# Performance work log

Measured on AMD Instinct MI355X. Metric: run time of the kernel, lower is better.

Reference implementation:

```python
import jax, jax.numpy as jnp
import numpy as np
from functools import partial

N_NODES = 50000


def gcn_conv(x, row, col, norm, W, b, num_nodes):
    # x: [N, Fin], W: [Fout, Fin] (torch Linear weight layout), b: [Fout]
    h = x @ W.T                                   # [N, Fout]
    msg = norm[:, None] * h[row]                  # per-edge message, gather x_j = x[row]
    out = jax.ops.segment_sum(msg, col, num_segments=num_nodes)  # scatter-add to target col
    return out + b


def _build_norm(row, col, edge_weight, num_nodes):
    # add self-loops with weight 1.0
    loops = jnp.arange(num_nodes, dtype=row.dtype)
    row_f = jnp.concatenate([row, loops])
    col_f = jnp.concatenate([col, loops])
    ew_f = jnp.concatenate([edge_weight, jnp.ones((num_nodes,), edge_weight.dtype)])
    # degree counts occurrences of row (unweighted, like PyG degree())
    deg = jax.ops.segment_sum(jnp.ones_like(ew_f), row_f, num_segments=num_nodes)
    dinv = jnp.where(deg > 0, deg ** -0.5, 0.0).astype(edge_weight.dtype)
    norm = dinv[row_f] * ew_f * dinv[col_f]
    return row_f, col_f, norm


def setup_inputs() -> dict:
    key = jax.random.key(0)
    k = jax.random.split(key, 8)
    N, E = N_NODES, 800000
    Fin, H, C = 256, 96, 40
    x = jax.random.normal(k[0], (N, Fin), dtype=jnp.float32)
    edge_index = jax.random.randint(k[1], (2, E), 0, N, dtype=jnp.int64)
    edge_weight = jax.random.uniform(k[2], (E,), dtype=jnp.float32)
    W1 = jax.random.normal(k[3], (H, Fin), dtype=jnp.float32) * (1.0 / np.sqrt(Fin))
    b1 = jnp.zeros((H,), jnp.float32)
    W2 = jax.random.normal(k[4], (C, H), dtype=jnp.float32) * (1.0 / np.sqrt(H))
    b2 = jnp.zeros((C,), jnp.float32)
    return {"x": x, "edge_index": edge_index, "edge_weight": edge_weight,
            "W1": W1, "b1": b1, "W2": W2, "b2": b2}


def reference(x, edge_index, edge_weight, W1, b1, W2, b2):
    N = x.shape[0]
    row, col = edge_index[0], edge_index[1]
    row_f, col_f, norm = _build_norm(row, col, edge_weight, N)
    h = jax.nn.relu(gcn_conv(x, row_f, col_f, norm, W1, b1, N))
    # dropout is identity in eval mode
    out = gcn_conv(h, row_f, col_f, norm, W2, b2, N)
    return jax.nn.log_softmax(out, axis=1)
```

## Files before the change

kernel.cpp:

```cpp
#include <hip/hip_runtime.h>
#include <hip/hip_bf16.h>
#include <hip/hip_fp16.h>
#include <math.h>

#define NN 50000
#define EE 800000
#define FIN 256
#define FH 96
#define FC 40
#define NBK 196

typedef _Float16 h4 __attribute__((ext_vector_type(4)));
typedef _Float16 h8 __attribute__((ext_vector_type(8)));
typedef float f32x4 __attribute__((ext_vector_type(4)));


__global__ __launch_bounds__(256) void k_hist(const int* __restrict__ ei, int E,
                                              unsigned* __restrict__ copies) {
    __shared__ unsigned hist[12500];
    int b = blockIdx.x;
    int slice = b & 63;
    int half = (b >> 6) & 1;
    int arr = b >> 7;
    const int* ptr = ei + (size_t)arr * E;
    int tid = threadIdx.x;
    for (int i = tid; i < 12500; i += 256) hist[i] = 0u;
    __syncthreads();
    int ES = (E + 63) >> 6;
    int lo = slice * ES, hi = min(lo + ES, E);
    int nlo = half * 25000;
    for (int i = lo + tid; i < hi; i += 256) {
        int rel = ptr[i] - nlo;
        if ((unsigned)rel < 25000u)
            atomicAdd(&hist[rel >> 1], 1u << ((rel & 1) << 4));
    }
    __syncthreads();
    unsigned* dst = copies + (size_t)((arr * 2 + half) * 64 + slice) * 12500;
    for (int i = tid; i < 12500; i += 256) dst[i] = hist[i];
}

__global__ void k_reduce(const unsigned* __restrict__ copies,
                         float* __restrict__ dinv, unsigned* __restrict__ cnt) {
    int t = blockIdx.x * blockDim.x + threadIdx.x;
    if (t >= 25000) return;
    int half = t / 12500, w = t - half * 12500;
    unsigned sr = 0, sc = 0;
    const unsigned* br = copies + (size_t)(half) * 64 * 12500 + w;
    const unsigned* bc = copies + (size_t)(2 + half) * 64 * 12500 + w;
#pragma unroll 8
    for (int s = 0; s < 64; ++s) { sr += br[s * 12500]; sc += bc[s * 12500]; }
    int n0 = half * 25000 + 2 * w;
    dinv[n0]     = rsqrtf((float)((sr & 0xffffu) + 1u));
    dinv[n0 + 1] = rsqrtf((float)((sr >> 16) + 1u));
    cnt[n0]     = sc & 0xffffu;
    cnt[n0 + 1] = sc >> 16;
}


__global__ __launch_bounds__(1024) void k_scanA(const unsigned* __restrict__ cnt,
                                                unsigned* __restrict__ off,
                                                unsigned* __restrict__ bsum, int n) {
    __shared__ unsigned s[1024];
    int t = threadIdx.x;
    int i = blockIdx.x * 1024 + t;
    unsigned v = (i < n) ? cnt[i] : 0u;
    s[t] = v;
    __syncthreads();
    for (int o = 1; o < 1024; o <<= 1) {
        unsigned tv = (t >= o) ? s[t - o] : 0u;
        __syncthreads();
        s[t] += tv;
        __syncthreads();
    }
    if (i < n) off[i] = s[t] - v;
    if (t == 1023) bsum[blockIdx.x] = s[1023];
}

__global__ void k_scanB1(unsigned* bsum, int nb) {
    if (threadIdx.x == 0 && blockIdx.x == 0) {
        unsigned run = 0;
        for (int b = 0; b < nb; ++b) { unsigned tv = bsum[b]; bsum[b] = run; run += tv; }
    }
}

__global__ void k_scanB2(unsigned* __restrict__ off, const unsigned* __restrict__ bsum,
                         unsigned* __restrict__ gcur, int n, unsigned e) {
    int i = blockIdx.x * blockDim.x + threadIdx.x;
    if (i < n) {
        unsigned v = off[i] + bsum[i >> 10];
        off[i] = v;
        if ((i & 255) == 0) gcur[i >> 8] = v;
    }
    if (i == n) off[n] = e;
}


__global__ __launch_bounds__(256) void k_bucket(const int* __restrict__ row,
                                                const int* __restrict__ col,
                                                const float* __restrict__ ew,
                                                unsigned* __restrict__ gcur,
                                                unsigned* __restrict__ bkc,
                                                float2* __restrict__ bkrw, int E) {
    __shared__ unsigned cnt[NBK];
    __shared__ unsigned cur[NBK];
    int tid = threadIdx.x;
    int CH = (E + gridDim.x - 1) / gridDim.x;
    int lo = blockIdx.x * CH, hi = min(lo + CH, E);
    for (int i = tid; i < NBK; i += 256) cnt[i] = 0u;
    __syncthreads();
    for (int i = lo + tid; i < hi; i += 256) atomicAdd(&cnt[col[i] >> 8], 1u);
    __syncthreads();
    for (int i = tid; i < NBK; i += 256) cur[i] = atomicAdd(&gcur[i], cnt[i]);
    __syncthreads();
    for (int i = lo + tid; i < hi; i += 256) {
        int c = col[i];
        unsigned pos = atomicAdd(&cur[c >> 8], 1u);
        bkc[pos] = (unsigned)c;
        float2 p;
        p.x = __int_as_float(row[i]);
        p.y = ew[i];
        bkrw[pos] = p;
    }
}


__global__ __launch_bounds__(256) void k_place(const unsigned* __restrict__ bkc,
                                               const float2* __restrict__ bkrw,
                                               const unsigned* __restrict__ off,
                                               float2* __restrict__ epk, int n) {
    __shared__ unsigned cur[256];
    int b = blockIdx.x;
    int tid = threadIdx.x;
    int node0 = b * 256;
    int node = node0 + tid;
    cur[tid] = off[(node <= n) ? node : n];
    __syncthreads();
    unsigned st = off[node0];
    unsigned en = off[min(node0 + 256, n)];
    for (unsigned i = st + tid; i < en; i += 256) {
        unsigned c = bkc[i];
        unsigned pos = atomicAdd(&cur[c & 255], 1u);
        epk[pos] = bkrw[i];
    }
}


__global__ __launch_bounds__(256) void k_gemm1(const float* __restrict__ x,
                                               const float* __restrict__ W,
                                               const float* __restrict__ dinv,
                                               _Float16* __restrict__ g0h, int n) {
    __shared__ _Float16 xs[64][72];
    __shared__ _Float16 wsm[96][72];
    int tid = threadIdx.x;
    int row0 = blockIdx.x * 64;
    int l = tid & 63, w = tid >> 6;
    int l15 = l & 15, lg = l >> 4;

    f32x4 acc[6];
#pragma unroll
    for (int c = 0; c < 6; ++c) acc[c] = (f32x4)0.f;

    for (int kc = 0; kc < 4; ++kc) {
        int kbase = kc * 64;
#pragma unroll
        for (int i = 0; i < 4; ++i) {
            int it = tid + 256 * i;
            int r = it >> 4, k4 = it & 15;
            float4 v = make_float4(0.f, 0.f, 0.f, 0.f);
            int gr = row0 + r;
            if (gr < n) v = *(const float4*)&x[gr * FIN + kbase + k4 * 4];
            h4 hv = {(_Float16)v.x, (_Float16)v.y, (_Float16)v.z, (_Float16)v.w};
            *(h4*)&xs[r][k4 * 4] = hv;
        }
#pragma unroll
        for (int i = 0; i < 6; ++i) {
            int it = tid + 256 * i;
            int r = it >> 4, k4 = it & 15;
            float4 v = *(const float4*)&W[r * FIN + kbase + k4 * 4];
            h4 hv = {(_Float16)v.x, (_Float16)v.y, (_Float16)v.z, (_Float16)v.w};
            *(h4*)&wsm[r][k4 * 4] = hv;
        }
        __syncthreads();
#pragma unroll
        for (int ks = 0; ks < 2; ++ks) {
            h8 a = *(const h8*)&xs[16 * w + l15][ks * 32 + lg * 8];
#pragma unroll
            for (int ct = 0; ct < 6; ++ct) {
                h8 b = *(const h8*)&wsm[ct * 16 + l15][ks * 32 + lg * 8];
                acc[ct] = __builtin_amdgcn_mfma_f32_16x16x32_f16(a, b, acc[ct], 0, 0, 0);
            }
        }
        __syncthreads();
    }
#pragma unroll
    for (int r = 0; r < 4; ++r) {
        int grow = row0 + 16 * w + lg * 4 + r;
        if (grow < n) {
            float dv = dinv[grow];
#pragma unroll
            for (int ct = 0; ct < 6; ++ct)
                g0h[(size_t)grow * FH + ct * 16 + l15] = (_Float16)(dv * acc[ct][r]);
        }
    }
}


__global__ __launch_bounds__(256) void k_agg96(const _Float16* __restrict__ g0h,
                                               const unsigned* __restrict__ off,
                                               const float2* __restrict__ epk,
                                               const float* __restrict__ dinv,
                                               const float* __restrict__ b,
                                               _Float16* __restrict__ outh, int n) {
    int tid = blockIdx.x * 256 + threadIdx.x;
    int node = tid / 12;
    int f8 = tid - node * 12;
    if (node >= n) return;
    const h8* gp = (const h8*)g0h;
    h8 self = gp[(size_t)node * 12 + f8];
    float acc[8];
#pragma unroll
    for (int j = 0; j < 8; ++j) acc[j] = (float)self[j];
    unsigned st = off[node], en = off[node + 1];
    unsigned e = st;
    for (; e + 4 <= en; e += 4) {
        float2 p0 = epk[e + 0], p1 = epk[e + 1], p2 = epk[e + 2], p3 = epk[e + 3];
        h8 ga = gp[(size_t)__float_as_int(p0.x) * 12 + f8];
        h8 gb = gp[(size_t)__float_as_int(p1.x) * 12 + f8];
        h8 gc = gp[(size_t)__float_as_int(p2.x) * 12 + f8];
        h8 gd = gp[(size_t)__float_as_int(p3.x) * 12 + f8];
#pragma unroll
        for (int j = 0; j < 8; ++j) acc[j] = fmaf(p0.y, (float)ga[j], acc[j]);
#pragma unroll
        for (int j = 0; j < 8; ++j) acc[j] = fmaf(p1.y, (float)gb[j], acc[j]);
#pragma unroll
        for (int j = 0; j < 8; ++j) acc[j] = fmaf(p2.y, (float)gc[j], acc[j]);
#pragma unroll
        for (int j = 0; j < 8; ++j) acc[j] = fmaf(p3.y, (float)gd[j], acc[j]);
    }
    for (; e < en; ++e) {
        float2 p = epk[e];
        h8 g = gp[(size_t)__float_as_int(p.x) * 12 + f8];
#pragma unroll
        for (int j = 0; j < 8; ++j) acc[j] = fmaf(p.y, (float)g[j], acc[j]);
    }
    float s = dinv[node];
    float4 bv0 = ((const float4*)b)[f8 * 2];
    float4 bv1 = ((const float4*)b)[f8 * 2 + 1];
    const float bb[8] = {bv0.x, bv0.y, bv0.z, bv0.w, bv1.x, bv1.y, bv1.z, bv1.w};
    h8 o;
#pragma unroll
    for (int j = 0; j < 8; ++j) o[j] = (_Float16)fmaxf(fmaf(s, acc[j], bb[j]), 0.f);
    *(h8*)&outh[(size_t)node * FH + f8 * 8] = o;
}


__global__ __launch_bounds__(256) void k_gemm2(const _Float16* __restrict__ h,
                                               const float* __restrict__ W2,
                                               const float* __restrict__ dinv,
                                               _Float16* __restrict__ g1h, int n) {
    __shared__ _Float16 hs[64][104];
    __shared__ _Float16 wsm[48][104];
    int tid = threadIdx.x;
    int row0 = blockIdx.x * 64;
    int l = tid & 63, w = tid >> 6;
    int l15 = l & 15, lg = l >> 4;

    f32x4 acc[3];
#pragma unroll
    for (int c = 0; c < 3; ++c) acc[c] = (f32x4)0.f;

#pragma unroll
    for (int i = 0; i < 6; ++i) {
        int it = tid + 256 * i;
        int r = it / 24, k4 = it - r * 24;
        int gr = row0 + r;
        h4 hv = {(_Float16)0.f, (_Float16)0.f, (_Float16)0.f, (_Float16)0.f};
        if (gr < n) hv = *(const h4*)&h[(size_t)gr * FH + k4 * 4];
        *(h4*)&hs[r][k4 * 4] = hv;
    }
#pragma unroll
    for (int i = 0; i < 5; ++i) {
        int it = tid + 256 * i;
        if (it < 1152) {
            int r = it / 24, k4 = it - r * 24;
            h4 hv = {(_Float16)0.f, (_Float16)0.f, (_Float16)0.f, (_Float16)0.f};
            if (r < FC) {
                float4 v = *(const float4*)&W2[r * FH + k4 * 4];
                hv[0] = (_Float16)v.x; hv[1] = (_Float16)v.y;
                hv[2] = (_Float16)v.z; hv[3] = (_Float16)v.w;
            }
            *(h4*)&wsm[r][k4 * 4] = hv;
        }
    }
    __syncthreads();
#pragma unroll
    for (int ks = 0; ks < 3; ++ks) {
        h8 a = *(const h8*)&hs[16 * w + l15][ks * 32 + lg * 8];
#pragma unroll
        for (int ct = 0; ct < 3; ++ct) {
            h8 b = *(const h8*)&wsm[ct * 16 + l15][ks * 32 + lg * 8];
            acc[ct] = __builtin_amdgcn_mfma_f32_16x16x32_f16(a, b, acc[ct], 0, 0, 0);
        }
    }
#pragma unroll
    for (int r = 0; r < 4; ++r) {
        int grow = row0 + 16 * w + lg * 4 + r;
        if (grow < n) {
            float dv = dinv[grow];
#pragma unroll
            for (int ct = 0; ct < 3; ++ct) {
                int colc = ct * 16 + l15;
                if (colc < FC)
                    g1h[(size_t)grow * FC + colc] = (_Float16)(dv * acc[ct][r]);
            }
        }
    }
}


__global__ __launch_bounds__(256) void k_agg40lsm(const _Float16* __restrict__ g1h,
                                                  const unsigned* __restrict__ off,
                                                  const float2* __restrict__ epk,
                                                  const float* __restrict__ dinv,
                                                  const float* __restrict__ b,
                                                  float* __restrict__ out, int n) {
    __shared__ float sm[50][41];
    int tid = threadIdx.x;
    int ln = tid / 5;
    int f8 = tid - ln * 5;
    int node = blockIdx.x * 50 + ln;
    bool active = (tid < 250) && (node < n);
    float acc[8];
#pragma unroll
    for (int j = 0; j < 8; ++j) acc[j] = 0.f;
    if (active) {
        const h8* gp = (const h8*)g1h;
        h8 self = gp[(size_t)node * 5 + f8];
#pragma unroll
        for (int j = 0; j < 8; ++j) acc[j] = (float)self[j];
        unsigned st = off[node], en = off[node + 1];
        unsigned e = st;
        for (; e + 4 <= en; e += 4) {
            float2 p0 = epk[e + 0], p1 = epk[e + 1], p2 = epk[e + 2], p3 = epk[e + 3];
            h8 ga = gp[(size_t)__float_as_int(p0.x) * 5 + f8];
            h8 gb = gp[(size_t)__float_as_int(p1.x) * 5 + f8];
            h8 gc = gp[(size_t)__float_as_int(p2.x) * 5 + f8];
            h8 gd = gp[(size_t)__float_as_int(p3.x) * 5 + f8];
#pragma unroll
            for (int j = 0; j < 8; ++j) acc[j] = fmaf(p0.y, (float)ga[j], acc[j]);
#pragma unroll
            for (int j = 0; j < 8; ++j) acc[j] = fmaf(p1.y, (float)gb[j], acc[j]);
#pragma unroll
            for (int j = 0; j < 8; ++j) acc[j] = fmaf(p2.y, (float)gc[j], acc[j]);
#pragma unroll
            for (int j = 0; j < 8; ++j) acc[j] = fmaf(p3.y, (float)gd[j], acc[j]);
        }
        for (; e < en; ++e) {
            float2 p = epk[e];
            h8 g = gp[(size_t)__float_as_int(p.x) * 5 + f8];
#pragma unroll
            for (int j = 0; j < 8; ++j) acc[j] = fmaf(p.y, (float)g[j], acc[j]);
        }
        float s = dinv[node];
        float4 bv0 = ((const float4*)b)[f8 * 2];
        float4 bv1 = ((const float4*)b)[f8 * 2 + 1];
        const float bb[8] = {bv0.x, bv0.y, bv0.z, bv0.w, bv1.x, bv1.y, bv1.z, bv1.w};
#pragma unroll
        for (int j = 0; j < 8; ++j) {
            acc[j] = fmaf(s, acc[j], bb[j]);
            sm[ln][f8 * 8 + j] = acc[j];
        }
    }
    __syncthreads();
    if (tid < 50) {
        int nd = blockIdx.x * 50 + tid;
        if (nd < n) {
            float m = -INFINITY;
#pragma unroll 8
            for (int j = 0; j < FC; ++j) m = fmaxf(m, sm[tid][j]);
            float sum = 0.f;
#pragma unroll 8
            for (int j = 0; j < FC; ++j) sum += expf(sm[tid][j] - m);
            sm[tid][40] = logf(sum) + m;
        }
    }
    __syncthreads();
    if (active) {
        float lse = sm[ln][40];
        float4 o0 = make_float4(acc[0] - lse, acc[1] - lse, acc[2] - lse, acc[3] - lse);
        float4 o1 = make_float4(acc[4] - lse, acc[5] - lse, acc[6] - lse, acc[7] - lse);
        *(float4*)&out[(size_t)node * FC + f8 * 8] = o0;
        *(float4*)&out[(size_t)node * FC + f8 * 8 + 4] = o1;
    }
}


extern "C" void kernel_launch(void* const* d_in, const int* in_sizes, int n_in,
                              void* d_out, int out_size, void* d_ws, size_t ws_size,
                              hipStream_t stream) {
    const float* x  = (const float*)d_in[0];
    const int*   ei = (const int*)d_in[1];
    const float* ew = (const float*)d_in[2];
    const float* W1 = (const float*)d_in[3];
    const float* b1 = (const float*)d_in[4];
    const float* W2 = (const float*)d_in[5];
    const float* b2 = (const float*)d_in[6];
    float* out = (float*)d_out;

    const int N = NN;
    const int E = in_sizes[1] / 2;
    const int* row = ei;
    const int* col = ei + E;

    float* ws = (float*)d_ws;
    float*    dinv   = (float*)(ws + 0);
    unsigned* cnt    = (unsigned*)(ws + 50176);
    unsigned* off    = (unsigned*)(ws + 100352);
    unsigned* bsum   = (unsigned*)(ws + 150656);
    unsigned* gcur   = (unsigned*)(ws + 150720);
    unsigned* copies = (unsigned*)(ws + 150976);
    unsigned* bkc    = (unsigned*)(ws + 150976);
    float2*   bkrw   = (float2*)(ws + 950976);
    _Float16* h      = (_Float16*)(ws + 150976);
    float2*   epk    = (float2*)(ws + 4950976);
    _Float16* g0h    = (_Float16*)(ws + 6550976);
    _Float16* g1h    = (_Float16*)(ws + 8950976);

    const int B = 256;
    const int NB_SCAN = (N + 1023) / 1024;

    hipLaunchKernelGGL(k_hist, dim3(256), dim3(B), 0, stream, ei, E, copies);
    hipLaunchKernelGGL(k_reduce, dim3((25000 + B - 1) / B), dim3(B), 0, stream, copies, dinv, cnt);

    hipLaunchKernelGGL(k_scanA, dim3(NB_SCAN), dim3(1024), 0, stream, cnt, off, bsum, N);
    hipLaunchKernelGGL(k_scanB1, dim3(1), dim3(64), 0, stream, bsum, NB_SCAN);
    hipLaunchKernelGGL(k_scanB2, dim3((N + 1 + B - 1) / B), dim3(B), 0, stream, off, bsum, gcur, N, (unsigned)E);

    hipLaunchKernelGGL(k_bucket, dim3(320), dim3(B), 0, stream, row, col, ew, gcur, bkc, bkrw, E);
    hipLaunchKernelGGL(k_place, dim3(NBK), dim3(B), 0, stream, bkc, bkrw, off, epk, N);

    hipLaunchKernelGGL(k_gemm1, dim3((N + 63) / 64), dim3(B), 0, stream, x, W1, dinv, g0h, N);

    hipLaunchKernelGGL(k_agg96, dim3((N * 12 + B - 1) / B), dim3(B), 0, stream,
                       g0h, off, epk, dinv, b1, h, N);

    hipLaunchKernelGGL(k_gemm2, dim3((N + 63) / 64), dim3(B), 0, stream, h, W2, dinv, g1h, N);

    hipLaunchKernelGGL(k_agg40lsm, dim3((N + 49) / 50), dim3(B), 0, stream,
                       g1h, off, epk, dinv, b2, out, N);
}
```

Baseline: 144.0 us.

## Replace global per-node col histogram and scan with bucket counts and local scans

Per-node column counts and the three-kernel global prefix scan are dropped. The histogram kernel now counts only per-bucket (256-node) column totals, k_reduce scans those 196 bucket counts, and k_place builds per-node CSR offsets inside each bucket with a local LDS histogram and scan. This removes the 64 column-histogram copies (their traffic and the reduction over them) and three kernel launches, at the cost of an extra read of bucketed columns in k_place and a memset.

```diff
diff --git a/kernel.cpp b/kernel.cpp
--- a/kernel.cpp
+++ b/kernel.cpp
@@ -15,83 +15,79 @@
 typedef float f32x4 __attribute__((ext_vector_type(4)));
 
 
-__global__ __launch_bounds__(256) void k_hist(const int* __restrict__ ei, int E,
-                                              unsigned* __restrict__ copies) {
-    __shared__ unsigned hist[12500];
+__global__ __launch_bounds__(256) void k_histcnt(const int* __restrict__ ei, int E,
+                                                 unsigned* __restrict__ copies,
+                                                 unsigned* __restrict__ bcnt) {
+    __shared__ unsigned lds[12500];
     int b = blockIdx.x;
-    int slice = b & 63;
-    int half = (b >> 6) & 1;
-    int arr = b >> 7;
-    const int* ptr = ei + (size_t)arr * E;
-    int tid = threadIdx.x;
-    for (int i = tid; i < 12500; i += 256) hist[i] = 0u;
-    __syncthreads();
+    int tid = threadIdx.x;
     int ES = (E + 63) >> 6;
-    int lo = slice * ES, hi = min(lo + ES, E);
-    int nlo = half * 25000;
-    for (int i = lo + tid; i < hi; i += 256) {
-        int rel = ptr[i] - nlo;
-        if ((unsigned)rel < 25000u)
-            atomicAdd(&hist[rel >> 1], 1u << ((rel & 1) << 4));
-    }
-    __syncthreads();
-    unsigned* dst = copies + (size_t)((arr * 2 + half) * 64 + slice) * 12500;
-    for (int i = tid; i < 12500; i += 256) dst[i] = hist[i];
-}
-
-__global__ void k_reduce(const unsigned* __restrict__ copies,
-                         float* __restrict__ dinv, unsigned* __restrict__ cnt) {
+    if (b < 128) {
+        int slice = b & 63, half = b >> 6;
+        const int* ptr = ei;
+        for (int i = tid; i < 12500; i += 256) lds[i] = 0u;
+        __syncthreads();
+        int lo = slice * ES, hi = min(lo + ES, E);
+        int nlo = half * 25000;
+        for (int i = lo + tid; i < hi; i += 256) {
+            int rel = ptr[i] - nlo;
+            if ((unsigned)rel < 25000u)
+                atomicAdd(&lds[rel >> 1], 1u << ((rel & 1) << 4));
+        }
+        __syncthreads();
+        unsigned* dst = copies + (size_t)(half * 64 + slice) * 12500;
+        for (int i = tid; i < 12500; i += 256) dst[i] = lds[i];
+    } else {
+        int chunk = b - 128;
+        const int* col = ei + E;
+        for (int i = tid; i < NBK; i += 256) lds[i] = 0u;
+        __syncthreads();
+        int lo = chunk * ES, hi = min(lo + ES, E);
+        for (int i = lo + tid; i < hi; i += 256) atomicAdd(&lds[col[i] >> 8], 1u);
+        __syncthreads();
+        for (int i = tid; i < NBK; i += 256)
+            if (lds[i]) atomicAdd(&bcnt[i], lds[i]);
+    }
+}
+
+
+__global__ __launch_bounds__(256) void k_reduce(const unsigned* __restrict__ copies,
+                                                const unsigned* __restrict__ bcnt,
+                                                float* __restrict__ dinv,
+                                                unsigned* __restrict__ bstart,
+                                                unsigned* __restrict__ gcur,
+                                                unsigned* __restrict__ off, unsigned E) {
     int t = blockIdx.x * blockDim.x + threadIdx.x;
-    if (t >= 25000) return;
-    int half = t / 12500, w = t - half * 12500;
-    unsigned sr = 0, sc = 0;
-    const unsigned* br = copies + (size_t)(half) * 64 * 12500 + w;
-    const unsigned* bc = copies + (size_t)(2 + half) * 64 * 12500 + w;
+    if (t < 25000) {
+        int half = t / 12500, w = t - half * 12500;
+        unsigned sr = 0;
+        const unsigned* br = copies + (size_t)half * 64 * 12500 + w;
 #pragma unroll 8
-    for (int s = 0; s < 64; ++s) { sr += br[s * 12500]; sc += bc[s * 12500]; }
-    int n0 = half * 25000 + 2 * w;
-    dinv[n0]     = rsqrtf((float)((sr & 0xffffu) + 1u));
-    dinv[n0 + 1] = rsqrtf((float)((sr >> 16) + 1u));
-    cnt[n0]     = sc & 0xffffu;
-    cnt[n0 + 1] = sc >> 16;
-}
-
-
-__global__ __launch_bounds__(1024) void k_scanA(const unsigned* __restrict__ cnt,
-                                                unsigned* __restrict__ off,
-                                                unsigned* __restrict__ bsum, int n) {
-    __shared__ unsigned s[1024];
-    int t = threadIdx.x;
-    int i = blockIdx.x * 1024 + t;
-    unsigned v = (i < n) ? cnt[i] : 0u;
-    s[t] = v;
-    __syncthreads();
-    for (int o = 1; o < 1024; o <<= 1) {
-        unsigned tv = (t >= o) ? s[t - o] : 0u;
-        __syncthreads();
-        s[t] += tv;
-        __syncthreads();
-    }
-    if (i < n) off[i] = s[t] - v;
-    if (t == 1023) bsum[blockIdx.x] = s[1023];
-}
-
-__global__ void k_scanB1(unsigned* bsum, int nb) {
-    if (threadIdx.x == 0 && blockIdx.x == 0) {
-        unsigned run = 0;
-        for (int b = 0; b < nb; ++b) { unsigned tv = bsum[b]; bsum[b] = run; run += tv; }
-    }
-}
-
-__global__ void k_scanB2(unsigned* __restrict__ off, const unsigned* __restrict__ bsum,
-                         unsigned* __restrict__ gcur, int n, unsigned e) {
-    int i = blockIdx.x * blockDim.x + threadIdx.x;
-    if (i < n) {
-        unsigned v = off[i] + bsum[i >> 10];
-        off[i] = v;
-        if ((i & 255) == 0) gcur[i >> 8] = v;
-    }
-    if (i == n) off[n] = e;
+        for (int s = 0; s < 64; ++s) sr += br[s * 12500];
+        int n0 = half * 25000 + 2 * w;
+        dinv[n0]     = rsqrtf((float)((sr & 0xffffu) + 1u));
+        dinv[n0 + 1] = rsqrtf((float)((sr >> 16) + 1u));
+    }
+    if (blockIdx.x == 0) {
+        __shared__ unsigned sb[256];
+        int tt = threadIdx.x;
+        unsigned v = (tt < NBK) ? bcnt[tt] : 0u;
+        sb[tt] = v;
+        __syncthreads();
+        for (int o = 1; o < 256; o <<= 1) {
+            unsigned tv = (tt >= o) ? sb[tt - o] : 0u;
+            __syncthreads();
+            sb[tt] += tv;
+            __syncthreads();
+        }
+        if (tt < NBK) {
+            unsigned ex = sb[tt] - v;
+            bstart[tt] = ex;
+            gcur[tt] = ex;
+            bstart[tt + 1] = sb[tt];
+        }
+        if (tt == 0) off[NN] = E;
+    }
 }
 
 
@@ -126,17 +122,33 @@
 
 __global__ __launch_bounds__(256) void k_place(const unsigned* __restrict__ bkc,
                                                const float2* __restrict__ bkrw,
-                                               const unsigned* __restrict__ off,
+                                               const unsigned* __restrict__ bstart,
+                                               unsigned* __restrict__ off,
                                                float2* __restrict__ epk, int n) {
+    __shared__ unsigned cnt[256];
     __shared__ unsigned cur[256];
     int b = blockIdx.x;
     int tid = threadIdx.x;
     int node0 = b * 256;
+    unsigned st = bstart[b], en = bstart[b + 1];
+    cnt[tid] = 0u;
+    __syncthreads();
+    for (unsigned i = st + tid; i < en; i += 256) atomicAdd(&cnt[bkc[i] & 255], 1u);
+    __syncthreads();
+    unsigned v = cnt[tid];
+    cur[tid] = v;
+    __syncthreads();
+    for (int o = 1; o < 256; o <<= 1) {
+        unsigned tv = (tid >= o) ? cur[tid - o] : 0u;
+        __syncthreads();
+        cur[tid] += tv;
+        __syncthreads();
+    }
+    unsigned base = st + cur[tid] - v;
     int node = node0 + tid;
-    cur[tid] = off[(node <= n) ? node : n];
-    __syncthreads();
-    unsigned st = off[node0];
-    unsigned en = off[min(node0 + 256, n)];
+    if (node < n) off[node] = base;
+    cur[tid] = base;
+    __syncthreads();
     for (unsigned i = st + tid; i < en; i += 256) {
         unsigned c = bkc[i];
         unsigned pos = atomicAdd(&cur[c & 255], 1u);
@@ -414,10 +426,10 @@
 
     float* ws = (float*)d_ws;
     float*    dinv   = (float*)(ws + 0);
-    unsigned* cnt    = (unsigned*)(ws + 50176);
-    unsigned* off    = (unsigned*)(ws + 100352);
-    unsigned* bsum   = (unsigned*)(ws + 150656);
-    unsigned* gcur   = (unsigned*)(ws + 150720);
+    unsigned* off    = (unsigned*)(ws + 50176);
+    unsigned* bcnt   = (unsigned*)(ws + 100480);
+    unsigned* bstart = (unsigned*)(ws + 100736);
+    unsigned* gcur   = (unsigned*)(ws + 100992);
     unsigned* copies = (unsigned*)(ws + 150976);
     unsigned* bkc    = (unsigned*)(ws + 150976);
     float2*   bkrw   = (float2*)(ws + 950976);
@@ -427,17 +439,15 @@
     _Float16* g1h    = (_Float16*)(ws + 8950976);
 
     const int B = 256;
-    const int NB_SCAN = (N + 1023) / 1024;
-
-    hipLaunchKernelGGL(k_hist, dim3(256), dim3(B), 0, stream, ei, E, copies);
-    hipLaunchKernelGGL(k_reduce, dim3((25000 + B - 1) / B), dim3(B), 0, stream, copies, dinv, cnt);
-
-    hipLaunchKernelGGL(k_scanA, dim3(NB_SCAN), dim3(1024), 0, stream, cnt, off, bsum, N);
-    hipLaunchKernelGGL(k_scanB1, dim3(1), dim3(64), 0, stream, bsum, NB_SCAN);
-    hipLaunchKernelGGL(k_scanB2, dim3((N + 1 + B - 1) / B), dim3(B), 0, stream, off, bsum, gcur, N, (unsigned)E);
+
+    hipMemsetAsync(bcnt, 0, 256 * sizeof(unsigned), stream);
+
+    hipLaunchKernelGGL(k_histcnt, dim3(192), dim3(B), 0, stream, ei, E, copies, bcnt);
+    hipLaunchKernelGGL(k_reduce, dim3(98), dim3(B), 0, stream,
+                       copies, bcnt, dinv, bstart, gcur, off, (unsigned)E);
 
     hipLaunchKernelGGL(k_bucket, dim3(320), dim3(B), 0, stream, row, col, ew, gcur, bkc, bkrw, E);
-    hipLaunchKernelGGL(k_place, dim3(NBK), dim3(B), 0, stream, bkc, bkrw, off, epk, N);
+    hipLaunchKernelGGL(k_place, dim3(NBK), dim3(B), 0, stream, bkc, bkrw, bstart, off, epk, N);
 
     hipLaunchKernelGGL(k_gemm1, dim3((N + 63) / 64), dim3(B), 0, stream, x, W1, dinv, g0h, N);
 
```

After: 142.2 us. About the same (-1.3%).
